# Performance work log

Measured on AMD Instinct MI355X. Metric: run time of the kernel, lower is better.

Reference implementation:

```python
import jax, jax.numpy as jnp
import numpy as np

N_FEATURES = 170
D_MODEL = 64
N_HEADS = 4
ALPHA = 0.1
LN_EPS = 1e-5
LEAKY_SLOPE = 0.01  # torch F.leaky_relu default
N = 3 * N_FEATURES  # 510
B = 32


def setup_inputs() -> dict:
    key = jax.random.key(0)
    ks = jax.random.split(key, 10)
    D, H = D_MODEL, N_HEADS
    s = 1.0 / np.sqrt(D)
    return {
        "x": jax.random.normal(ks[0], (B, N, D), dtype=jnp.float32),
        "causal_graph": jax.random.uniform(ks[1], (N, N), dtype=jnp.float32),
        # nn.Linear(d_model, d_model*n_heads, bias=False): stored here as (D, H*D) for x @ W
        "W": jax.random.uniform(ks[2], (D, H * D), jnp.float32, -s, s),
        "attention_w": jax.random.normal(ks[3], (H, 2 * D), dtype=jnp.float32),
        # Conv2d(2, n_heads, 3, padding=1): OIHW kernel
        "conv_w": jax.random.uniform(ks[4], (H, 2, 3, 3), jnp.float32, -1/np.sqrt(18), 1/np.sqrt(18)),
        "conv_b": jax.random.uniform(ks[5], (H,), jnp.float32, -1/np.sqrt(18), 1/np.sqrt(18)),
        # nn.Linear(d_model, 2*d_model): stored as (D, 2D)
        "fcg_w": jax.random.uniform(ks[6], (D, 2 * D), jnp.float32, -s, s),
        "fcg_b": jax.random.uniform(ks[7], (2 * D,), jnp.float32, -s, s),
        "ln_g": jnp.ones((D,), jnp.float32),
        "ln_b": jnp.zeros((D,), jnp.float32),
    }


def reference(x, causal_graph, W, attention_w, conv_w, conv_b, fcg_w, fcg_b, ln_g, ln_b):
    Bz, Nn, D = x.shape
    H = N_HEADS
    # shared projection: (B, N, H, D)
    xt = (x @ W).reshape(Bz, Nn, H, D)
    # GAT-style additive scores: concat-dot decomposed into two dot products
    w1, w2 = attention_w[:, :D], attention_w[:, D:]  # each (H, D)
    s_i = jnp.einsum('bnhd,hd->bhn', xt, w1)  # source term
    s_j = jnp.einsum('bnhd,hd->bhn', xt, w2)  # target term
    e = s_i[:, :, :, None] + s_j[:, :, None, :]  # (B, H, N, N)
    A_eva = jnp.where(e >= 0, e, LEAKY_SLOPE * e)  # leaky_relu
    # fuse mean attention with causal graph via 3x3 conv
    A_mean = A_eva.mean(axis=1)  # (B, N, N)
    causal = jnp.broadcast_to(causal_graph[None], (Bz, Nn, Nn))
    stacked = jnp.stack([A_mean, causal], axis=1)  # (B, 2, N, N)
    A_st = jax.lax.conv_general_dilated(
        stacked, conv_w, window_strides=(1, 1), padding=((1, 1), (1, 1)),
        dimension_numbers=('NCHW', 'OIHW', 'NCHW'))
    A_st = A_st + conv_b[None, :, None, None]  # (B, H, N, N)
    A = jax.nn.softmax(ALPHA * A_eva + (1.0 - ALPHA) * A_st, axis=-1)
    # multi-head aggregation then head-mean
    out = jnp.einsum('bhnm,bmhd->bnhd', A, xt).mean(axis=2)  # (B, N, D)
    # GLU
    g = out @ fcg_w + fcg_b  # (B, N, 2D)
    a, b = g[..., :D], g[..., D:]
    glu = a * jax.nn.sigmoid(b)
    # residual + layernorm
    y = glu + x
    mu = y.mean(axis=-1, keepdims=True)
    var = ((y - mu) ** 2).mean(axis=-1, keepdims=True)
    y = (y - mu) * jax.lax.rsqrt(var + LN_EPS) * ln_g + ln_b
    return y, A
```

## Files before the change

### kernel.cpp

```cpp
#include <hip/hip_runtime.h>

#define Bz 32
#define Nn 510
#define Dd 64
#define Hh 4
#define HD_ 256
#define Kpad 512
#define ALPHA_ 0.1f
#define LNEPS 1e-5f
#define SLOPE 0.01f
#define NEG_INF -3.0e38f

typedef __attribute__((ext_vector_type(8))) short short8;
typedef __attribute__((ext_vector_type(4))) float floatx4;

__device__ inline float wredsum(float v) {
  #pragma unroll
  for (int off = 32; off; off >>= 1) v += __shfl_xor(v, off, 64);
  return v;
}
__device__ inline float wredmax(float v) {
  #pragma unroll
  for (int off = 32; off; off >>= 1) v = fmaxf(v, __shfl_xor(v, off, 64));
  return v;
}
__device__ inline unsigned short f2bf(float f) {
  unsigned int u = __float_as_uint(f);
  unsigned int r = (u + 0x7fffu + ((u >> 16) & 1u)) >> 16;
  return (unsigned short)r;
}

__global__ __launch_bounds__(256) void k1_xt(const float* __restrict__ x,
                                             const float* __restrict__ W,
                                             const float* __restrict__ attw,
                                             unsigned short* __restrict__ xtT,
                                             float* __restrict__ si,
                                             float* __restrict__ sj) {
  __shared__ float Wl[64][68];
  __shared__ float xr[32][68];
  __shared__ unsigned short st[64 * 33];
  const int t = threadIdx.x;
  const int rt = blockIdx.x;
  const int b = blockIdx.y;
  const int ch = blockIdx.z;
  #pragma unroll
  for (int k = 0; k < 4; k++) {
    int f = t + k * 256;
    int kr = f >> 4;
    int c = (f & 15) * 4;
    *(float4*)&Wl[kr][c] = *(const float4*)&W[kr * HD_ + ch * 64 + c];
  }
  #pragma unroll
  for (int k = 0; k < 2; k++) {
    int f = t + k * 256;
    int r = f >> 4;
    int c = (f & 15) * 4;
    int row = rt * 32 + r;
    float4 v = make_float4(0.f, 0.f, 0.f, 0.f);
    if (row < Nn) v = *(const float4*)&x[(b * Nn + row) * Dd + c];
    *(float4*)&xr[r][c] = v;
  }
  __syncthreads();
  const int tg = t >> 4;
  const int tc = t & 15;
  const int rb = tg * 2, c0 = tc * 4;
  float acc[2][4] = {};
  #pragma unroll
  for (int k4 = 0; k4 < 16; k4++) {
    float4 xv0 = *(float4*)&xr[rb][k4 * 4];
    float4 xv1 = *(float4*)&xr[rb + 1][k4 * 4];
    #pragma unroll
    for (int kk = 0; kk < 4; kk++) {
      float4 wv = *(float4*)&Wl[k4 * 4 + kk][c0];
      float xs0 = (&xv0.x)[kk];
      float xs1 = (&xv1.x)[kk];
      acc[0][0] = fmaf(xs0, wv.x, acc[0][0]);
      acc[0][1] = fmaf(xs0, wv.y, acc[0][1]);
      acc[0][2] = fmaf(xs0, wv.z, acc[0][2]);
      acc[0][3] = fmaf(xs0, wv.w, acc[0][3]);
      acc[1][0] = fmaf(xs1, wv.x, acc[1][0]);
      acc[1][1] = fmaf(xs1, wv.y, acc[1][1]);
      acc[1][2] = fmaf(xs1, wv.z, acc[1][2]);
      acc[1][3] = fmaf(xs1, wv.w, acc[1][3]);
    }
  }
  #pragma unroll
  for (int cc = 0; cc < 4; cc++) {
    #pragma unroll
    for (int r = 0; r < 2; r++) {
      st[(c0 + cc) * 33 + rb + r] = f2bf(acc[r][cc]);
    }
  }
  float w1v[4], w2v[4];
  #pragma unroll
  for (int cc = 0; cc < 4; cc++) {
    w1v[cc] = attw[ch * 128 + c0 + cc];
    w2v[cc] = attw[ch * 128 + 64 + c0 + cc];
  }
  #pragma unroll
  for (int r = 0; r < 2; r++) {
    float p1 = acc[r][0] * w1v[0] + acc[r][1] * w1v[1] +
               acc[r][2] * w1v[2] + acc[r][3] * w1v[3];
    float p2 = acc[r][0] * w2v[0] + acc[r][1] * w2v[1] +
               acc[r][2] * w2v[2] + acc[r][3] * w2v[3];
    #pragma unroll
    for (int off = 1; off <= 8; off <<= 1) {
      p1 += __shfl_xor(p1, off, 64);
      p2 += __shfl_xor(p2, off, 64);
    }
    if (tc == 0) {
      int row = rt * 32 + rb + r;
      if (row < Nn) {
        si[(b * 4 + ch) * Nn + row] = p1;
        sj[(b * 4 + ch) * Nn + row] = p2;
      }
    }
  }
  __syncthreads();
  if (t < 64) {
    unsigned short* dst = &xtT[((size_t)(b * 4 + ch) * 64 + t) * Kpad + rt * 32];
    #pragma unroll
    for (int q = 0; q < 4; q++) {
      short8 v;
      #pragma unroll
      for (int k = 0; k < 8; k++) v[k] = (short)st[t * 33 + q * 8 + k];
      *(short8*)&dst[q * 8] = v;
    }
  }
}

__global__ __launch_bounds__(256) void k2_attn(const float* __restrict__ si,
                                               const float* __restrict__ sj,
                                               const float* __restrict__ causal,
                                               const float* __restrict__ convw,
                                               const float* __restrict__ convb,
                                               float* __restrict__ A) {
  __shared__ float am_t[10 * 8 * 68];
  __shared__ float cz_t[10 * 8 * 68];
  __shared__ float sjl[4 * 8 * 68];
  __shared__ float sil[4][12];
  const int t = threadIdx.x;
  const int i0 = blockIdx.x * 8;
  const int b = blockIdx.y;
  if (t < 40) {
    int h = t / 10, r = t % 10;
    int iq = i0 + r - 1;
    sil[h][r] = (iq >= 0 && iq < Nn) ? si[(b * 4 + h) * Nn + iq] : 0.f;
  }
  if (t >= 64 && t < 224) {
    int q = t - 64;
    int r = q >> 4, rem = q & 15;
    int e = rem >> 1, side = rem & 1;
    int idx = (r * 8 + e) * 68 + side * 65;
    am_t[idx] = 0.f;
    cz_t[idx] = 0.f;
  }
  for (int f = t; f < 2048; f += 256) {
    int h = f >> 9, j = f & 511;
    float v = (j < Nn) ? sj[(b * 4 + h) * Nn + j] : 0.f;
    sjl[(h * 8 + (j & 7)) * 68 + (j >> 3) + 1] = v;
  }
  __syncthreads();
  for (int f = t; f < 5120; f += 256) {
    int r = f >> 9, j = f & 511;
    int iq = i0 + r - 1;
    float am = 0.f, cz = 0.f;
    if (iq >= 0 && iq < Nn && j < Nn) {
      float s = 0.f;
      #pragma unroll
      for (int h = 0; h < 4; h++) {
        float e2 = sil[h][r] + sjl[(h * 8 + (j & 7)) * 68 + (j >> 3) + 1];
        s += (e2 >= 0.f) ? e2 : SLOPE * e2;
      }
      am = 0.25f * s;
      cz = causal[iq * Nn + j];
    }
    int idx = (r * 8 + (j & 7)) * 68 + (j >> 3) + 1;
    am_t[idx] = am;
    cz_t[idx] = cz;
  }
  __syncthreads();
  const int w = t >> 6, L = t & 63;
  const int j0 = L * 8;
  for (int pp = w; pp < 32; pp += 4) {
    const int il = pp >> 2, h = pp & 3;
    const int i = i0 + il;
    if (i >= Nn) continue;
    const int bh = b * 4 + h;
    const float sih = sil[h][il + 1];
    float cw[18];
    #pragma unroll
    for (int q = 0; q < 18; q++) cw[q] = convw[h * 18 + q];
    const float cb = convb[h];
    float conv[8];
    #pragma unroll
    for (int e = 0; e < 8; e++) conv[e] = cb;
    #pragma unroll
    for (int r3 = 0; r3 < 3; r3++) {
      const float* ba = &am_t[((il + r3) * 8) * 68];
      const float* bc = &cz_t[((il + r3) * 8) * 68];
      float a[10], c[10];
      a[0] = ba[7 * 68 + L];
      c[0] = bc[7 * 68 + L];
      #pragma unroll
      for (int e = 0; e < 8; e++) {
        a[1 + e] = ba[e * 68 + L + 1];
        c[1 + e] = bc[e * 68 + L + 1];
      }
      a[9] = ba[0 * 68 + L + 2];
      c[9] = bc[0 * 68 + L + 2];
      float w0 = cw[r3 * 3], w1 = cw[r3 * 3 + 1], w2 = cw[r3 * 3 + 2];
      float u0 = cw[9 + r3 * 3], u1 = cw[9 + r3 * 3 + 1], u2 = cw[9 + r3 * 3 + 2];
      #pragma unroll
      for (int e = 0; e < 8; e++) {
        float cv = conv[e];
        cv = fmaf(w0, a[e], cv);
        cv = fmaf(w1, a[e + 1], cv);
        cv = fmaf(w2, a[e + 2], cv);
        cv = fmaf(u0, c[e], cv);
        cv = fmaf(u1, c[e + 1], cv);
        cv = fmaf(u2, c[e + 2], cv);
        conv[e] = cv;
      }
    }
    float v[8];
    float mx = NEG_INF;
    #pragma unroll
    for (int e = 0; e < 8; e++) {
      float ee = sih + sjl[(h * 8 + e) * 68 + L + 1];
      float l = (ee >= 0.f) ? ee : SLOPE * ee;
      float val = ALPHA_ * l + (1.0f - ALPHA_) * conv[e];
      v[e] = (j0 + e < Nn) ? val : NEG_INF;
      mx = fmaxf(mx, v[e]);
    }
    mx = wredmax(mx);
    float p[8], s = 0.f;
    #pragma unroll
    for (int e = 0; e < 8; e++) {
      p[e] = __expf(v[e] - mx);
      s += p[e];
    }
    s = wredsum(s);
    const float inv = 1.f / s;
    #pragma unroll
    for (int e = 0; e < 8; e++) p[e] *= inv;
    float* Ar = &A[((size_t)bh * Nn + i) * Nn + j0];
    *(float4*)&Ar[0] = make_float4(p[0], p[1], p[2], p[3]);
    if (L < 63) {
      *(float4*)&Ar[4] = make_float4(p[4], p[5], p[6], p[7]);
    } else {
      *(float2*)&Ar[4] = make_float2(p[4], p[5]);
    }
  }
}

__global__ __launch_bounds__(256) void k3_out(const float* __restrict__ A,
                                              const unsigned short* __restrict__ xtT,
                                              const float* __restrict__ x,
                                              const float* __restrict__ fcgw,
                                              const float* __restrict__ fcgb,
                                              const float* __restrict__ lng,
                                              const float* __restrict__ lnb,
                                              float* __restrict__ y) {
  __shared__ unsigned short Asub[2][16 * 72];
  __shared__ float ol[16][64];
  __shared__ float gl[2][128];
  const int t = threadIdx.x;
  const int n0 = blockIdx.x * 16;
  const int b = blockIdx.y;
  const int w = t >> 6, L = t & 63;
  const int quad = L >> 4, l16 = L & 15;
  const int wc = w * 16;
  const int ar = t >> 4;
  const int amc = (t & 15) * 4;
  const int nrow = n0 + ar;
  floatx4 acc = {0.f, 0.f, 0.f, 0.f};

  auto stage = [&](int p) {
    const int h = p >> 3;
    const int m = (p & 7) * 64 + amc;
    float av[4] = {0.f, 0.f, 0.f, 0.f};
    if (nrow < Nn) {
      const float* src = &A[((size_t)(b * 4 + h) * Nn + nrow) * Nn + m];
      if (m + 3 < Nn) {
        float2 v0 = *(const float2*)&src[0];
        float2 v1 = *(const float2*)&src[2];
        av[0] = v0.x; av[1] = v0.y; av[2] = v1.x; av[3] = v1.y;
      } else {
        int lim = Nn - m;
        #pragma unroll
        for (int q = 0; q < 4; q++) if (q < lim) av[q] = src[q];
      }
    }
    ushort4 u;
    u.x = f2bf(av[0]); u.y = f2bf(av[1]);
    u.z = f2bf(av[2]); u.w = f2bf(av[3]);
    *(ushort4*)&Asub[p & 1][ar * 72 + amc] = u;
  };

  stage(0);
  __syncthreads();
  #pragma unroll 2
  for (int p = 0; p < 32; p++) {
    if (p + 1 < 32) stage(p + 1);
    const int h = p >> 3;
    const unsigned short* Xr =
        &xtT[((size_t)(b * 4 + h) * 64 + wc + l16) * Kpad + (p & 7) * 64];
    short8 af0 = *(short8*)&Asub[p & 1][l16 * 72 + quad * 8];
    short8 bf0 = *(const short8*)&Xr[quad * 8];
    acc = __builtin_amdgcn_mfma_f32_16x16x32_bf16(af0, bf0, acc, 0, 0, 0);
    short8 af1 = *(short8*)&Asub[p & 1][l16 * 72 + 32 + quad * 8];
    short8 bf1 = *(const short8*)&Xr[32 + quad * 8];
    acc = __builtin_amdgcn_mfma_f32_16x16x32_bf16(af1, bf1, acc, 0, 0, 0);
    __syncthreads();
  }

  #pragma unroll
  for (int reg = 0; reg < 4; reg++) {
    ol[quad * 4 + reg][wc + l16] = 0.25f * acc[reg];
  }
  __syncthreads();
  const int kk = t & 127;
  const int rg = t >> 7;
  for (int it = 0; it < 8; it++) {
    const int r = it * 2 + rg;
    const int row = n0 + r;
    float g = fcgb[kk];
    #pragma unroll
    for (int d = 0; d < 64; d++) g = fmaf(ol[r][d], fcgw[d * 128 + kk], g);
    gl[rg][kk] = g;
    __syncthreads();
    if (kk < 64 && row < Nn) {
      float a = gl[rg][kk];
      float bb = gl[rg][kk + 64];
      float glu = a / (1.f + __expf(-bb));
      float yv = glu + x[(b * Nn + row) * Dd + kk];
      float mu = wredsum(yv) * (1.f / 64.f);
      float dv = yv - mu;
      float var = wredsum(dv * dv) * (1.f / 64.f);
      float o = dv * rsqrtf(var + LNEPS) * lng[kk] + lnb[kk];
      y[(b * Nn + row) * Dd + kk] = o;
    }
    __syncthreads();
  }
}

extern "C" void kernel_launch(void* const* d_in, const int* in_sizes, int n_in,
                              void* d_out, int out_size, void* d_ws, size_t ws_size,
                              hipStream_t stream) {
  const float* x      = (const float*)d_in[0];
  const float* causal = (const float*)d_in[1];
  const float* W      = (const float*)d_in[2];
  const float* attw   = (const float*)d_in[3];
  const float* convw  = (const float*)d_in[4];
  const float* convb  = (const float*)d_in[5];
  const float* fcgw   = (const float*)d_in[6];
  const float* fcgb   = (const float*)d_in[7];
  const float* lng    = (const float*)d_in[8];
  const float* lnb    = (const float*)d_in[9];

  float* ws = (float*)d_ws;
  float* si = ws;
  float* sj = si + (size_t)Bz * Hh * Nn;
  unsigned short* xtT = (unsigned short*)(sj + (size_t)Bz * Hh * Nn + 16);

  float* yout = (float*)d_out;
  float* Aout = yout + (size_t)Bz * Nn * Dd;

  k1_xt  <<<dim3(16, Bz, 4), 256, 0, stream>>>(x, W, attw, xtT, si, sj);
  k2_attn<<<dim3(64, Bz), 256, 0, stream>>>(si, sj, causal, convw, convb, Aout);
  k3_out <<<dim3(32, Bz), 256, 0, stream>>>(Aout, xtT, x, fcgw, fcgb, lng, lnb, yout);
}
```

Before: 274.0 us.

## Precompute batch-invariant causal-graph conv once and reuse across batches and heads

The causal channel of the 3x3 conv does not depend on the batch, so a new kernel computes its contribution plus bias once per head into a workspace buffer. The attention kernel then reads that precomputed term with vector loads instead of staging the causal tile in shared memory and convolving it for every batch. It also restructures each wave to handle two rows across all four heads, so the attention tile's conv taps are loaded once per row and shared across heads. This adds an extra launch, a 4×510×512 float workspace, and an extra global read per output, in exchange for fewer shared-memory loads and FMAs.

```diff
diff --git a/kernel.cpp b/kernel.cpp
--- a/kernel.cpp
+++ b/kernel.cpp
@@ -129,19 +129,49 @@
   }
 }
 
+__global__ __launch_bounds__(256) void k2a_cconv(const float* __restrict__ causal,
+                                                 const float* __restrict__ convw,
+                                                 const float* __restrict__ convb,
+                                                 float* __restrict__ ccv) {
+  const int i = blockIdx.x;
+  const int t = threadIdx.x;
+  #pragma unroll
+  for (int qq = 0; qq < 2; qq++) {
+    const int j = t + qq * 256;
+    float tap[9];
+    #pragma unroll
+    for (int r3 = 0; r3 < 3; r3++) {
+      int ii = i - 1 + r3;
+      #pragma unroll
+      for (int c3 = 0; c3 < 3; c3++) {
+        int jj = j - 1 + c3;
+        tap[r3 * 3 + c3] = (ii >= 0 && ii < Nn && jj >= 0 && jj < Nn)
+                               ? causal[ii * Nn + jj] : 0.f;
+      }
+    }
+    #pragma unroll
+    for (int h = 0; h < 4; h++) {
+      float acc = convb[h];
+      #pragma unroll
+      for (int q = 0; q < 9; q++) acc = fmaf(convw[h * 18 + 9 + q], tap[q], acc);
+      ccv[((size_t)h * Nn + i) * 512 + j] = acc;
+    }
+  }
+}
+
 __global__ __launch_bounds__(256) void k2_attn(const float* __restrict__ si,
                                                const float* __restrict__ sj,
-                                               const float* __restrict__ causal,
+                                               const float* __restrict__ ccv,
                                                const float* __restrict__ convw,
-                                               const float* __restrict__ convb,
                                                float* __restrict__ A) {
   __shared__ float am_t[10 * 8 * 68];
-  __shared__ float cz_t[10 * 8 * 68];
   __shared__ float sjl[4 * 8 * 68];
   __shared__ float sil[4][12];
+  __shared__ float cwl[4][9];
   const int t = threadIdx.x;
   const int i0 = blockIdx.x * 8;
   const int b = blockIdx.y;
+  if (t < 36) cwl[t / 9][t % 9] = convw[(t / 9) * 18 + (t % 9)];
   if (t < 40) {
     int h = t / 10, r = t % 10;
     int iq = i0 + r - 1;
@@ -151,9 +181,7 @@
     int q = t - 64;
     int r = q >> 4, rem = q & 15;
     int e = rem >> 1, side = rem & 1;
-    int idx = (r * 8 + e) * 68 + side * 65;
-    am_t[idx] = 0.f;
-    cz_t[idx] = 0.f;
+    am_t[(r * 8 + e) * 68 + side * 65] = 0.f;
   }
   for (int f = t; f < 2048; f += 256) {
     int h = f >> 9, j = f & 511;
@@ -164,7 +192,7 @@
   for (int f = t; f < 5120; f += 256) {
     int r = f >> 9, j = f & 511;
     int iq = i0 + r - 1;
-    float am = 0.f, cz = 0.f;
+    float am = 0.f;
     if (iq >= 0 && iq < Nn && j < Nn) {
       float s = 0.f;
       #pragma unroll
@@ -173,83 +201,78 @@
         s += (e2 >= 0.f) ? e2 : SLOPE * e2;
       }
       am = 0.25f * s;
-      cz = causal[iq * Nn + j];
-    }
-    int idx = (r * 8 + (j & 7)) * 68 + (j >> 3) + 1;
-    am_t[idx] = am;
-    cz_t[idx] = cz;
+    }
+    am_t[(r * 8 + (j & 7)) * 68 + (j >> 3) + 1] = am;
   }
   __syncthreads();
   const int w = t >> 6, L = t & 63;
   const int j0 = L * 8;
-  for (int pp = w; pp < 32; pp += 4) {
-    const int il = pp >> 2, h = pp & 3;
+  #pragma unroll
+  for (int qq = 0; qq < 2; qq++) {
+    const int il = w * 2 + qq;
     const int i = i0 + il;
     if (i >= Nn) continue;
-    const int bh = b * 4 + h;
-    const float sih = sil[h][il + 1];
-    float cw[18];
-    #pragma unroll
-    for (int q = 0; q < 18; q++) cw[q] = convw[h * 18 + q];
-    const float cb = convb[h];
-    float conv[8];
-    #pragma unroll
-    for (int e = 0; e < 8; e++) conv[e] = cb;
+    float conv[4][8];
+    #pragma unroll
+    for (int h = 0; h < 4; h++) {
+      const float* cp = &ccv[((size_t)h * Nn + i) * 512 + j0];
+      float4 c0 = *(const float4*)&cp[0];
+      float4 c1 = *(const float4*)&cp[4];
+      conv[h][0] = c0.x; conv[h][1] = c0.y; conv[h][2] = c0.z; conv[h][3] = c0.w;
+      conv[h][4] = c1.x; conv[h][5] = c1.y; conv[h][6] = c1.z; conv[h][7] = c1.w;
+    }
     #pragma unroll
     for (int r3 = 0; r3 < 3; r3++) {
       const float* ba = &am_t[((il + r3) * 8) * 68];
-      const float* bc = &cz_t[((il + r3) * 8) * 68];
-      float a[10], c[10];
+      float a[10];
       a[0] = ba[7 * 68 + L];
-      c[0] = bc[7 * 68 + L];
+      #pragma unroll
+      for (int e = 0; e < 8; e++) a[1 + e] = ba[e * 68 + L + 1];
+      a[9] = ba[0 * 68 + L + 2];
+      #pragma unroll
+      for (int h = 0; h < 4; h++) {
+        float w0 = cwl[h][r3 * 3], w1 = cwl[h][r3 * 3 + 1], w2 = cwl[h][r3 * 3 + 2];
+        #pragma unroll
+        for (int e = 0; e < 8; e++) {
+          float cv = conv[h][e];
+          cv = fmaf(w0, a[e], cv);
+          cv = fmaf(w1, a[e + 1], cv);
+          cv = fmaf(w2, a[e + 2], cv);
+          conv[h][e] = cv;
+        }
+      }
+    }
+    #pragma unroll
+    for (int h = 0; h < 4; h++) {
+      const float sih = sil[h][il + 1];
+      float v[8];
+      float mx = NEG_INF;
       #pragma unroll
       for (int e = 0; e < 8; e++) {
-        a[1 + e] = ba[e * 68 + L + 1];
-        c[1 + e] = bc[e * 68 + L + 1];
-      }
-      a[9] = ba[0 * 68 + L + 2];
-      c[9] = bc[0 * 68 + L + 2];
-      float w0 = cw[r3 * 3], w1 = cw[r3 * 3 + 1], w2 = cw[r3 * 3 + 2];
-      float u0 = cw[9 + r3 * 3], u1 = cw[9 + r3 * 3 + 1], u2 = cw[9 + r3 * 3 + 2];
+        float ee = sih + sjl[(h * 8 + e) * 68 + L + 1];
+        float l = (ee >= 0.f) ? ee : SLOPE * ee;
+        float val = ALPHA_ * l + (1.0f - ALPHA_) * conv[h][e];
+        v[e] = (j0 + e < Nn) ? val : NEG_INF;
+        mx = fmaxf(mx, v[e]);
+      }
+      mx = wredmax(mx);
+      float p[8], s = 0.f;
       #pragma unroll
       for (int e = 0; e < 8; e++) {
-        float cv = conv[e];
-        cv = fmaf(w0, a[e], cv);
-        cv = fmaf(w1, a[e + 1], cv);
-        cv = fmaf(w2, a[e + 2], cv);
-        cv = fmaf(u0, c[e], cv);
-        cv = fmaf(u1, c[e + 1], cv);
-        cv = fmaf(u2, c[e + 2], cv);
-        conv[e] = cv;
-      }
-    }
-    float v[8];
-    float mx = NEG_INF;
-    #pragma unroll
-    for (int e = 0; e < 8; e++) {
-      float ee = sih + sjl[(h * 8 + e) * 68 + L + 1];
-      float l = (ee >= 0.f) ? ee : SLOPE * ee;
-      float val = ALPHA_ * l + (1.0f - ALPHA_) * conv[e];
-      v[e] = (j0 + e < Nn) ? val : NEG_INF;
-      mx = fmaxf(mx, v[e]);
-    }
-    mx = wredmax(mx);
-    float p[8], s = 0.f;
-    #pragma unroll
-    for (int e = 0; e < 8; e++) {
-      p[e] = __expf(v[e] - mx);
-      s += p[e];
-    }
-    s = wredsum(s);
-    const float inv = 1.f / s;
-    #pragma unroll
-    for (int e = 0; e < 8; e++) p[e] *= inv;
-    float* Ar = &A[((size_t)bh * Nn + i) * Nn + j0];
-    *(float4*)&Ar[0] = make_float4(p[0], p[1], p[2], p[3]);
-    if (L < 63) {
-      *(float4*)&Ar[4] = make_float4(p[4], p[5], p[6], p[7]);
-    } else {
-      *(float2*)&Ar[4] = make_float2(p[4], p[5]);
+        p[e] = __expf(v[e] - mx);
+        s += p[e];
+      }
+      s = wredsum(s);
+      const float inv = 1.f / s;
+      #pragma unroll
+      for (int e = 0; e < 8; e++) p[e] *= inv;
+      float* Ar = &A[((size_t)(b * 4 + h) * Nn + i) * Nn + j0];
+      *(float4*)&Ar[0] = make_float4(p[0], p[1], p[2], p[3]);
+      if (L < 63) {
+        *(float4*)&Ar[4] = make_float4(p[4], p[5], p[6], p[7]);
+      } else {
+        *(float2*)&Ar[4] = make_float2(p[4], p[5]);
+      }
     }
   }
 }
@@ -363,11 +386,13 @@
   float* si = ws;
   float* sj = si + (size_t)Bz * Hh * Nn;
   unsigned short* xtT = (unsigned short*)(sj + (size_t)Bz * Hh * Nn + 16);
+  float* ccv = (float*)(xtT + (size_t)Bz * Hh * Dd * Kpad);
 
   float* yout = (float*)d_out;
   float* Aout = yout + (size_t)Bz * Nn * Dd;
 
+  k2a_cconv<<<dim3(Nn), 256, 0, stream>>>(causal, convw, convb, ccv);
   k1_xt  <<<dim3(16, Bz, 4), 256, 0, stream>>>(x, W, attw, xtT, si, sj);
-  k2_attn<<<dim3(64, Bz), 256, 0, stream>>>(si, sj, causal, convw, convb, Aout);
+  k2_attn<<<dim3(64, Bz), 256, 0, stream>>>(si, sj, ccv, convw, Aout);
   k3_out <<<dim3(32, Bz), 256, 0, stream>>>(Aout, xtT, x, fcgw, fcgb, lng, lnb, yout);
 }
```

Measured after the change: 260.5 us. 1.05x faster.
